# Kernel optimization log

Hardware: AMD Instinct MI355X
Metric: run time of the kernel (lower is better)

Reference implementation:

```python
import jax, jax.numpy as jnp
import numpy as np

HEADS = 8
DIM_HEAD = 32
DIM = 256
HIDDEN = HEADS * DIM_HEAD  # 256


def setup_inputs() -> dict:
    key = jax.random.key(0)
    ks = jax.random.split(key, 6)
    B, T, C, H, W = 4, 16, DIM, 32, 32
    x = jax.random.normal(ks[0], (B, T, C, H, W), dtype=jnp.float32)
    rel_pos = jax.random.normal(ks[1], (HEADS, T, T), dtype=jnp.float32)
    # 1x1 conv weights == channel-mixing matrices
    w_qkv = jax.random.normal(ks[2], (3 * HIDDEN, C), dtype=jnp.float32) * (C ** -0.5)
    b_qkv = jnp.zeros((3 * HIDDEN,), dtype=jnp.float32)
    w_out = jax.random.normal(ks[3], (C, HIDDEN), dtype=jnp.float32) * (HIDDEN ** -0.5)
    b_out = jnp.zeros((C,), dtype=jnp.float32)
    return {"x": x, "rel_pos": rel_pos, "w_qkv": w_qkv, "b_qkv": b_qkv,
            "w_out": w_out, "b_out": b_out}


def reference(x, rel_pos, w_qkv, b_qkv, w_out, b_out):
    B, T, C, H, W = x.shape
    scale = DIM_HEAD ** -0.5
    # 1x1 conv QKV projection: (B,T,C,H,W) x (3*hidden, C) -> (B,T,H,W,3*hidden)
    qkv = jnp.einsum('btchw,oc->bthwo', x, w_qkv) + b_qkv
    q, k, v = jnp.split(qkv, 3, axis=-1)
    # split heads: (B,T,H,W,heads,dim_head); attention over T per (b,h,w,head)
    q = q.reshape(B, T, H, W, HEADS, DIM_HEAD) * scale
    k = k.reshape(B, T, H, W, HEADS, DIM_HEAD)
    v = v.reshape(B, T, H, W, HEADS, DIM_HEAD)
    # sim: (B,H,W,heads,T,T)
    sim = jnp.einsum('bihwnd,bjhwnd->bhwnij', q, k)
    sim = sim + rel_pos  # (heads,T,T) broadcasts over (B,H,W)
    attn = jax.nn.softmax(sim, axis=-1)
    out = jnp.einsum('bhwnij,bjhwnd->bihwnd', attn, v)  # (B,T,H,W,heads,dh)
    out = out.reshape(B, T, H, W, HIDDEN)
    # 1x1 conv output projection back to C channels
    y = jnp.einsum('bthwe,ce->bthwc', out, w_out) + b_out
    return jnp.transpose(y, (0, 1, 4, 2, 3))  # (B,T,C,H,W)
```

## Files before the change

kernel.cpp:

```cpp
#include <hip/hip_runtime.h>
#include <hip/hip_bf16.h>

typedef __attribute__((ext_vector_type(8))) short bf16x8;
typedef __attribute__((ext_vector_type(4))) float f32x4;
typedef __attribute__((ext_vector_type(16))) float f32x16;

namespace {

constexpr int kT = 16;
constexpr int kC = 256;
constexpr int kHW = 1024;

__device__ __forceinline__ unsigned short f2bf(float f) {
  unsigned int x;
  __builtin_memcpy(&x, &f, 4);
  x += 0x7fff + ((x >> 16) & 1);
  return (unsigned short)(x >> 16);
}
__device__ __forceinline__ unsigned int pack2(float a, float b) {
  return (unsigned int)f2bf(a) | ((unsigned int)f2bf(b) << 16);
}

__global__ __launch_bounds__(256) void prep(const float* __restrict__ x,
                                            const float* __restrict__ wqkv,
                                            const float* __restrict__ wout,
                                            unsigned short* __restrict__ xT,
                                            unsigned short* __restrict__ wAll) {
  __shared__ unsigned short ts[64 * 72];
  const int bx = blockIdx.x;
  const int tid = threadIdx.x;
  if (bx < 4096) {
    const int cc = bx & 3, hc = (bx >> 2) & 15, t = (bx >> 6) & 15, b = bx >> 10;
    const int c0 = cc * 64, hw0 = hc * 64;
    {
      const int ci = tid >> 2, j = tid & 3;
      const float* xrow = x + (((size_t)(b * 16 + t) * 256 + c0 + ci) * 1024) + hw0;
#pragma unroll
      for (int u = 0; u < 4; ++u) {
        const int chunk = j + u * 4;
        const float4 v = *(const float4*)(xrow + chunk * 4);
        const int hwl = chunk * 4;
        ts[(hwl + 0) * 72 + ci] = f2bf(v.x);
        ts[(hwl + 1) * 72 + ci] = f2bf(v.y);
        ts[(hwl + 2) * 72 + ci] = f2bf(v.z);
        ts[(hwl + 3) * 72 + ci] = f2bf(v.w);
      }
    }
    __syncthreads();
    {
      const int hwp = tid >> 2, jp = tid & 3;
      const uint4 a = *(const uint4*)&ts[hwp * 72 + jp * 16];
      const uint4 bq = *(const uint4*)&ts[hwp * 72 + jp * 16 + 8];
      unsigned short* dst =
          xT + ((size_t)((b * 1024 + hw0 + hwp) * 16 + t) * 256) + c0 + jp * 16;
      *(uint4*)dst = a;
      *(uint4*)(dst + 8) = bq;
    }
  } else {
    const int g = bx - 4096;
    const int row_l = tid >> 3;
    const int seg = tid & 7;
    const float* src;
    int srow;
    if (g < 24) { src = wqkv; srow = (g % 3) * 256 + (g / 3) * 32 + row_l; }
    else        { src = wout; srow = (g - 24) * 32 + row_l; }
    const float* s = src + (size_t)srow * 256 + seg * 32;
    unsigned short* d = wAll + ((size_t)(g * 32 + row_l)) * 256 + seg * 32;
#pragma unroll
    for (int u = 0; u < 8; ++u) {
      const float4 v = *(const float4*)(s + u * 4);
      uint2 p;
      p.x = pack2(v.x, v.y);
      p.y = pack2(v.z, v.w);
      *(uint2*)(d + u * 4) = p;
    }
  }
}

constexpr int kWBStride = 264;
constexpr int kWBTile = 32 * kWBStride;
constexpr int kWB = 2 * kWBTile;
constexpr int kSite = 1824;
constexpr int kSmem = kWB + 8 * kSite;
static_assert(kSmem * 2 <= 65536, "LDS budget");

__global__ __launch_bounds__(512, 2) void attn_main(
    const unsigned short* __restrict__ xT,
    const float* __restrict__ rel,
    const unsigned short* __restrict__ wAll,
    const float* __restrict__ bqkv,
    const float* __restrict__ bout,
    float* __restrict__ out) {
  __shared__ __align__(16) unsigned short smem[kSmem];
  const int tid = threadIdx.x;
  const int lane = tid & 63;
  const int wave = tid >> 6;
  const int quad = lane >> 4;
  const int lrow = lane & 15;
  const int half = lane >> 5;
  const int n32 = lane & 31;
  const int b = blockIdx.x >> 6;
  const int hw0 = (blockIdx.x & 63) * 16;
  const int site0 = hw0 + wave * 2;

  bf16x8 ax[16];
  {
    const unsigned short* xs =
        xT + (((size_t)(b * 1024 + site0 + (n32 >> 4))) << 12) + lrow * 256;
#pragma unroll
    for (int ks = 0; ks < 16; ++ks)
      ax[ks] = *(const bf16x8*)(xs + ks * 16 + half * 8);
  }

  unsigned short* qb = smem + kWB + wave * kSite;
  unsigned short* kb = qb + 640;
  unsigned short* vt = qb + 1280;

  const int stageDst = (tid >> 4) * kWBStride + (tid & 15) * 16;
  const int stageSrcOff = (tid >> 4) * 256 + (tid & 15) * 16;

  uint4 pr0, pr1;
  {
    const unsigned short* sp = wAll + stageSrcOff;
    pr0 = *(const uint4*)sp;
    pr1 = *(const uint4*)(sp + 8);
  }

  const f32x4 zero4 = {0.f, 0.f, 0.f, 0.f};
  const float scale = 0.17677669529663687f;
  bf16x8 ao[2][8];

  auto qkv_tile = [&](int g, float bias) -> f32x16 {
    __syncthreads();
    unsigned short* WBc = smem + (g & 1) * kWBTile;
    *(uint4*)(WBc + stageDst) = pr0;
    *(uint4*)(WBc + stageDst + 8) = pr1;
    {
      const unsigned short* sp = wAll + (size_t)(g + 1) * 32 * 256 + stageSrcOff;
      pr0 = *(const uint4*)sp;
      pr1 = *(const uint4*)(sp + 8);
    }
    __syncthreads();
    f32x16 acc;
#pragma unroll
    for (int i = 0; i < 16; ++i) acc[i] = bias;
    const unsigned short* br = WBc + n32 * kWBStride + half * 8;
#pragma unroll
    for (int ks = 0; ks < 16; ++ks) {
      const bf16x8 bf = *(const bf16x8*)(br + ks * 16);
      acc = __builtin_amdgcn_mfma_f32_32x32x16_bf16(ax[ks], bf, acc, 0, 0, 0);
    }
    return acc;
  };

#pragma unroll 1
  for (int h = 0; h < 8; ++h) {
    const f32x16 qacc = qkv_tile(h * 3 + 0, bqkv[h * 32 + n32]);
    const f32x16 kacc = qkv_tile(h * 3 + 1, bqkv[256 + h * 32 + n32]);
    const f32x16 vacc = qkv_tile(h * 3 + 2, bqkv[512 + h * 32 + n32]);
    float rl[4];
#pragma unroll
    for (int r = 0; r < 4; ++r) rl[r] = rel[h * 256 + (quad * 4 + r) * 16 + lrow];

#pragma unroll
    for (int s = 0; s < 2; ++s) {
#pragma unroll
      for (int rr = 0; rr < 8; ++rr) {
        const int t = (rr & 3) + 8 * (rr >> 2) + 4 * half;
        qb[t * 40 + n32] = f2bf(qacc[8 * s + rr]);
        kb[t * 40 + n32] = f2bf(kacc[8 * s + rr]);
      }
#pragma unroll
      for (int rp = 0; rp < 4; ++rp) {
        const int rr = rp * 2;
        const int t = (rr & 3) + 8 * (rr >> 2) + 4 * half;
        *(unsigned int*)&vt[n32 * 16 + t] =
            pack2(vacc[8 * s + rr], vacc[8 * s + rr + 1]);
      }
      const bf16x8 qf = *(const bf16x8*)(qb + lrow * 40 + quad * 8);
      const bf16x8 kf = *(const bf16x8*)(kb + lrow * 40 + quad * 8);
      const f32x4 sim = __builtin_amdgcn_mfma_f32_16x16x32_bf16(qf, kf, zero4, 0, 0, 0);
      float p[4], inv[4];
#pragma unroll
      for (int r = 0; r < 4; ++r) {
        const float v = sim[r] * scale + rl[r];
        float m = v;
        for (int off = 8; off; off >>= 1) m = fmaxf(m, __shfl_xor(m, off));
        const float e = __expf(v - m);
        float sum = e;
        for (int off = 8; off; off >>= 1) sum += __shfl_xor(sum, off);
        p[r] = e;
        inv[r] = 1.0f / sum;
      }
      unsigned short* pb = kb;
#pragma unroll
      for (int r = 0; r < 4; ++r) pb[(quad * 4 + r) * 24 + lrow] = f2bf(p[r]);
      bf16x8 pf, vf0, vf1;
      if (quad < 2) {
        pf = *(const bf16x8*)(pb + lrow * 24 + quad * 8);
        vf0 = *(const bf16x8*)(vt + lrow * 16 + quad * 8);
        vf1 = *(const bf16x8*)(vt + (16 + lrow) * 16 + quad * 8);
      } else {
#pragma unroll
        for (int j = 0; j < 8; ++j) { pf[j] = 0; vf0[j] = 0; vf1[j] = 0; }
      }
      const f32x4 o0 = __builtin_amdgcn_mfma_f32_16x16x32_bf16(pf, vf0, zero4, 0, 0, 0);
      const f32x4 o1 = __builtin_amdgcn_mfma_f32_16x16x32_bf16(pf, vf1, zero4, 0, 0, 0);
#pragma unroll
      for (int r = 0; r < 4; ++r) {
        const int t = quad * 4 + r;
        qb[t * 40 + lrow] = f2bf(o0[r] * inv[r]);
        qb[t * 40 + 16 + lrow] = f2bf(o1[r] * inv[r]);
      }
      ao[s][h] = *(const bf16x8*)(qb + lrow * 40 + quad * 8);
    }
  }

  __syncthreads();
  float* fbuf = (float*)smem;
  float* ob = out + ((size_t)b << 22);
#pragma unroll 1
  for (int cc = 0; cc < 8; ++cc) {
#pragma unroll
    for (int sub = 0; sub < 2; ++sub) {
      const int c = cc * 32 + sub * 16 + lrow;
      const float bias = bout[c];
      f32x4 y0 = {bias, bias, bias, bias};
      f32x4 y1 = {bias, bias, bias, bias};
#pragma unroll
      for (int ks = 0; ks < 8; ++ks) {
        const bf16x8 wf =
            *(const bf16x8*)(wAll + (size_t)(768 + c) * 256 + ks * 32 + quad * 8);
        y0 = __builtin_amdgcn_mfma_f32_16x16x32_bf16(ao[0][ks], wf, y0, 0, 0, 0);
        y1 = __builtin_amdgcn_mfma_f32_16x16x32_bf16(ao[1][ks], wf, y1, 0, 0, 0);
      }
#pragma unroll
      for (int r = 0; r < 4; ++r) {
        const int t = quad * 4 + r;
        const int L = (t * 32 + sub * 16 + lrow) * 17 + wave * 2;
        fbuf[L] = y0[r];
        fbuf[L + 1] = y1[r];
      }
    }
    __syncthreads();
    {
      const int t = tid >> 5, cl = tid & 31;
      float v[16];
#pragma unroll
      for (int i = 0; i < 16; ++i) v[i] = fbuf[tid * 17 + i];
      float* dst = ob + ((size_t)(t * 256 + cc * 32 + cl)) * 1024 + hw0;
#pragma unroll
      for (int u = 0; u < 4; ++u) {
        float4 q;
        q.x = v[u * 4]; q.y = v[u * 4 + 1]; q.z = v[u * 4 + 2]; q.w = v[u * 4 + 3];
        *(float4*)(dst + u * 4) = q;
      }
    }
    __syncthreads();
  }
}

constexpr int kHWT = 4;
constexpr int kXsTStride = kC * kHWT + 8;
constexpr int kXSize = kT * kXsTStride;
constexpr int kWsOff = kXSize;
constexpr int kWsStride = 264;
constexpr int kWsSize = 32 * kWsStride;
constexpr int kQbOff = kWsOff + kWsSize;
constexpr int kQbWave = 1792;
constexpr int kLdsElems = kQbOff + 4 * kQbWave;

__global__ __launch_bounds__(256, 2) void fused_temporal_attn(
    const float* __restrict__ x, const float* __restrict__ rel,
    const float* __restrict__ wqkv, const float* __restrict__ bqkv,
    const float* __restrict__ wout, const float* __restrict__ bout,
    float* __restrict__ out) {
  __shared__ __align__(16) unsigned short smem[kLdsElems];
  const int tid = threadIdx.x;
  const int lane = tid & 63;
  const int wave = tid >> 6;
  const int quad = lane >> 4;
  const int lrow = lane & 15;
  const int b = blockIdx.x >> 8;
  const int tile = blockIdx.x & 255;
  const int hw0 = tile * kHWT;
  {
    const float* xb = x + (size_t)b * kT * kC * kHW + hw0;
#pragma unroll
    for (int it = 0; it < 16; ++it) {
      int idx = it * 256 + tid;
      int t = idx >> 8, c = idx & 255;
      const float4 v = *(const float4*)(xb + (size_t)(t * kC + c) * kHW);
      uint2 p;
      p.x = pack2(v.x, v.y);
      p.y = pack2(v.z, v.w);
      *(uint2*)&smem[t * kXsTStride + c * kHWT] = p;
    }
  }
  __syncthreads();
  bf16x8 ax[8];
#pragma unroll
  for (int ks = 0; ks < 8; ++ks) {
    bf16x8 f;
#pragma unroll
    for (int j = 0; j < 8; ++j) {
      int c = ks * 32 + quad * 8 + j;
      f[j] = (short)smem[lrow * kXsTStride + c * kHWT + wave];
    }
    ax[ks] = f;
  }
  unsigned short* qb = &smem[kQbOff + wave * kQbWave];
  unsigned short* kbuf = qb + 512;
  unsigned short* vtb = qb + 1024;
  unsigned short* pb = qb + 1536;
  const f32x4 zero4 = {0.f, 0.f, 0.f, 0.f};
  bf16x8 ao[8];
  for (int head = 0; head < 8; ++head) {
    for (int sel = 0; sel < 3; ++sel) {
      __syncthreads();
      {
        const float* wbp = wqkv + (size_t)(sel * 256 + head * 32) * kC;
#pragma unroll
        for (int i = 0; i < 8; ++i) {
          int seg = i * 256 + tid;
          int d = seg >> 6, s = seg & 63;
          const float4 v = *(const float4*)(wbp + d * kC + s * 4);
          uint2 p;
          p.x = pack2(v.x, v.y);
          p.y = pack2(v.z, v.w);
          *(uint2*)&smem[kWsOff + d * kWsStride + s * 4] = p;
        }
      }
      __syncthreads();
      float bias0 = bqkv[sel * 256 + head * 32 + lrow];
      float bias1 = bqkv[sel * 256 + head * 32 + 16 + lrow];
      f32x4 acc0 = {bias0, bias0, bias0, bias0};
      f32x4 acc1 = {bias1, bias1, bias1, bias1};
#pragma unroll
      for (int ks = 0; ks < 8; ++ks) {
        bf16x8 b0 = *(const bf16x8*)&smem[kWsOff + lrow * kWsStride + ks * 32 + quad * 8];
        bf16x8 b1 = *(const bf16x8*)&smem[kWsOff + (16 + lrow) * kWsStride + ks * 32 + quad * 8];
        acc0 = __builtin_amdgcn_mfma_f32_16x16x32_bf16(ax[ks], b0, acc0, 0, 0, 0);
        acc1 = __builtin_amdgcn_mfma_f32_16x16x32_bf16(ax[ks], b1, acc1, 0, 0, 0);
      }
      if (sel < 2) {
        unsigned short* dst = sel ? kbuf : qb;
#pragma unroll
        for (int r = 0; r < 4; ++r) {
          int row = quad * 4 + r;
          dst[row * 32 + lrow] = f2bf(acc0[r]);
          dst[row * 32 + 16 + lrow] = f2bf(acc1[r]);
        }
      } else {
#pragma unroll
        for (int r = 0; r < 4; ++r) {
          int row = quad * 4 + r;
          vtb[lrow * 16 + row] = f2bf(acc0[r]);
          vtb[(16 + lrow) * 16 + row] = f2bf(acc1[r]);
        }
      }
    }
    bf16x8 qf = *(const bf16x8*)&qb[lrow * 32 + quad * 8];
    bf16x8 kf = *(const bf16x8*)&kbuf[lrow * 32 + quad * 8];
    f32x4 sim = __builtin_amdgcn_mfma_f32_16x16x32_bf16(qf, kf, zero4, 0, 0, 0);
    const float scale = 0.17677669529663687f;
    float p[4], rsum[4];
#pragma unroll
    for (int r = 0; r < 4; ++r) {
      int i = quad * 4 + r;
      float v = sim[r] * scale + rel[head * 256 + i * 16 + lrow];
      float m = v;
      for (int off = 8; off; off >>= 1) m = fmaxf(m, __shfl_xor(m, off));
      float e = __expf(v - m);
      float s = e;
      for (int off = 8; off; off >>= 1) s += __shfl_xor(s, off);
      p[r] = e;
      rsum[r] = s;
    }
#pragma unroll
    for (int r = 0; r < 4; ++r) pb[(quad * 4 + r) * 16 + lrow] = f2bf(p[r]);
    bf16x8 pf, vf0, vf1;
    if (quad < 2) {
      pf = *(const bf16x8*)&pb[lrow * 16 + quad * 8];
      vf0 = *(const bf16x8*)&vtb[lrow * 16 + quad * 8];
      vf1 = *(const bf16x8*)&vtb[(16 + lrow) * 16 + quad * 8];
    } else {
#pragma unroll
      for (int j = 0; j < 8; ++j) { pf[j] = 0; vf0[j] = 0; vf1[j] = 0; }
    }
    f32x4 o0 = __builtin_amdgcn_mfma_f32_16x16x32_bf16(pf, vf0, zero4, 0, 0, 0);
    f32x4 o1 = __builtin_amdgcn_mfma_f32_16x16x32_bf16(pf, vf1, zero4, 0, 0, 0);
#pragma unroll
    for (int r = 0; r < 4; ++r) {
      int t = quad * 4 + r;
      float inv = 1.0f / rsum[r];
      qb[t * 32 + lrow] = f2bf(o0[r] * inv);
      qb[t * 32 + 16 + lrow] = f2bf(o1[r] * inv);
    }
    ao[head] = *(const bf16x8*)&qb[lrow * 32 + quad * 8];
  }
  float* ob = out + (size_t)b * kT * kC * kHW + hw0 + wave;
#pragma unroll 1
  for (int nt = 0; nt < 16; ++nt) {
    int c = nt * 16 + lrow;
    float bias = bout[c];
    f32x4 y = {bias, bias, bias, bias};
#pragma unroll
    for (int ks = 0; ks < 8; ++ks) {
      const float4 w0 = *(const float4*)(wout + (size_t)c * kC + ks * 32 + quad * 8);
      const float4 w1 = *(const float4*)(wout + (size_t)c * kC + ks * 32 + quad * 8 + 4);
      bf16x8 wf;
      wf[0] = (short)f2bf(w0.x); wf[1] = (short)f2bf(w0.y);
      wf[2] = (short)f2bf(w0.z); wf[3] = (short)f2bf(w0.w);
      wf[4] = (short)f2bf(w1.x); wf[5] = (short)f2bf(w1.y);
      wf[6] = (short)f2bf(w1.z); wf[7] = (short)f2bf(w1.w);
      y = __builtin_amdgcn_mfma_f32_16x16x32_bf16(ao[ks], wf, y, 0, 0, 0);
    }
#pragma unroll
    for (int r = 0; r < 4; ++r) {
      int t = quad * 4 + r;
      ob[(size_t)(t * kC + c) * kHW] = y[r];
    }
  }
}

}

extern "C" void kernel_launch(void* const* d_in, const int* in_sizes, int n_in,
                              void* d_out, int out_size, void* d_ws, size_t ws_size,
                              hipStream_t stream) {
  const float* x = (const float*)d_in[0];
  const float* rel = (const float*)d_in[1];
  const float* wqkv = (const float*)d_in[2];
  const float* bqkv = (const float*)d_in[3];
  const float* wout = (const float*)d_in[4];
  const float* bout = (const float*)d_in[5];
  float* out = (float*)d_out;
  (void)in_sizes; (void)n_in; (void)out_size;

  constexpr size_t kXTElems = (size_t)4 * 1024 * 16 * 256;
  constexpr size_t kWAllElems = 1024 * 256;
  constexpr size_t kNeed = (kXTElems + kWAllElems) * sizeof(unsigned short);

  if (ws_size >= kNeed) {
    unsigned short* xT = (unsigned short*)d_ws;
    unsigned short* wAll = xT + kXTElems;
    prep<<<4096 + 32, 256, 0, stream>>>(x, wqkv, wout, xT, wAll);
    attn_main<<<256, 512, 0, stream>>>(xT, rel, wAll, bqkv, bout, out);
  } else {
    fused_temporal_attn<<<1024, 256, 0, stream>>>(x, rel, wqkv, bqkv, wout, bout, out);
  }
}
```

Measured before the change: 243.6 us.

## Halve sites per wave in attn_main, use 16x16 MFMA and nontemporal loads/stores

Each wave now handles one spatial site instead of two, so the grid doubles to 512 blocks and launch bounds request 4 blocks per CU. The QKV projection switches from one 32x32x16 MFMA per k-step to two 16x16x32 MFMAs, which cuts accumulator and fragment register use. The aim is more parallelism and occupancy for a grid that was previously only 256 blocks. Nontemporal loads and stores are also added for the x input, the xT fragments and the output writes. In exchange, each block amortises its weight staging over half as many sites, so weight traffic through LDS doubles, and output stores become 32-byte chunks per row.

```diff
diff --git a/kernel.cpp b/kernel.cpp
--- a/kernel.cpp
+++ b/kernel.cpp
@@ -3,7 +3,7 @@
 
 typedef __attribute__((ext_vector_type(8))) short bf16x8;
 typedef __attribute__((ext_vector_type(4))) float f32x4;
-typedef __attribute__((ext_vector_type(16))) float f32x16;
+typedef __attribute__((ext_vector_type(4))) unsigned int uint4v;
 
 namespace {
 
@@ -19,6 +19,15 @@
 }
 __device__ __forceinline__ unsigned int pack2(float a, float b) {
   return (unsigned int)f2bf(a) | ((unsigned int)f2bf(b) << 16);
+}
+__device__ __forceinline__ bf16x8 ntload8(const unsigned short* p) {
+  uint4v v = __builtin_nontemporal_load((const uint4v*)p);
+  bf16x8 r;
+  __builtin_memcpy(&r, &v, 16);
+  return r;
+}
+__device__ __forceinline__ f32x4 ntload4f(const float* p) {
+  return __builtin_nontemporal_load((const f32x4*)p);
 }
 
 __global__ __launch_bounds__(256) void prep(const float* __restrict__ x,
@@ -38,7 +47,7 @@
 #pragma unroll
       for (int u = 0; u < 4; ++u) {
         const int chunk = j + u * 4;
-        const float4 v = *(const float4*)(xrow + chunk * 4);
+        const f32x4 v = ntload4f(xrow + chunk * 4);
         const int hwl = chunk * 4;
         ts[(hwl + 0) * 72 + ci] = f2bf(v.x);
         ts[(hwl + 1) * 72 + ci] = f2bf(v.y);
@@ -84,7 +93,9 @@
 constexpr int kSmem = kWB + 8 * kSite;
 static_assert(kSmem * 2 <= 65536, "LDS budget");
 
-__global__ __launch_bounds__(512, 2) void attn_main(
+struct Acc2 { f32x4 a0, a1; };
+
+__global__ __launch_bounds__(512, 4) void attn_main(
     const unsigned short* __restrict__ xT,
     const float* __restrict__ rel,
     const unsigned short* __restrict__ wAll,
@@ -97,19 +108,15 @@
   const int wave = tid >> 6;
   const int quad = lane >> 4;
   const int lrow = lane & 15;
-  const int half = lane >> 5;
-  const int n32 = lane & 31;
-  const int b = blockIdx.x >> 6;
-  const int hw0 = (blockIdx.x & 63) * 16;
-  const int site0 = hw0 + wave * 2;
-
-  bf16x8 ax[16];
+  const int b = blockIdx.x >> 7;
+  const int hw0 = (blockIdx.x & 127) * 8;
+  const int site = hw0 + wave;
+
+  bf16x8 ax[8];
   {
-    const unsigned short* xs =
-        xT + (((size_t)(b * 1024 + site0 + (n32 >> 4))) << 12) + lrow * 256;
-#pragma unroll
-    for (int ks = 0; ks < 16; ++ks)
-      ax[ks] = *(const bf16x8*)(xs + ks * 16 + half * 8);
+    const unsigned short* xs = xT + (((size_t)(b * 1024 + site)) << 12) + lrow * 256;
+#pragma unroll
+    for (int ks = 0; ks < 8; ++ks) ax[ks] = ntload8(xs + ks * 32 + quad * 8);
   }
 
   unsigned short* qb = smem + kWB + wave * kSite;
@@ -128,9 +135,9 @@
 
   const f32x4 zero4 = {0.f, 0.f, 0.f, 0.f};
   const float scale = 0.17677669529663687f;
-  bf16x8 ao[2][8];
-
-  auto qkv_tile = [&](int g, float bias) -> f32x16 {
+  bf16x8 ao[8];
+
+  auto qkv_tile = [&](int g, float bias0, float bias1) -> Acc2 {
     __syncthreads();
     unsigned short* WBc = smem + (g & 1) * kWBTile;
     *(uint4*)(WBc + stageDst) = pr0;
@@ -141,79 +148,85 @@
       pr1 = *(const uint4*)(sp + 8);
     }
     __syncthreads();
-    f32x16 acc;
-#pragma unroll
-    for (int i = 0; i < 16; ++i) acc[i] = bias;
-    const unsigned short* br = WBc + n32 * kWBStride + half * 8;
-#pragma unroll
-    for (int ks = 0; ks < 16; ++ks) {
-      const bf16x8 bf = *(const bf16x8*)(br + ks * 16);
-      acc = __builtin_amdgcn_mfma_f32_32x32x16_bf16(ax[ks], bf, acc, 0, 0, 0);
+    Acc2 acc;
+    acc.a0 = f32x4{bias0, bias0, bias0, bias0};
+    acc.a1 = f32x4{bias1, bias1, bias1, bias1};
+    const unsigned short* br0 = WBc + lrow * kWBStride + quad * 8;
+    const unsigned short* br1 = WBc + (16 + lrow) * kWBStride + quad * 8;
+#pragma unroll
+    for (int ks = 0; ks < 8; ++ks) {
+      const bf16x8 b0 = *(const bf16x8*)(br0 + ks * 32);
+      const bf16x8 b1 = *(const bf16x8*)(br1 + ks * 32);
+      acc.a0 = __builtin_amdgcn_mfma_f32_16x16x32_bf16(ax[ks], b0, acc.a0, 0, 0, 0);
+      acc.a1 = __builtin_amdgcn_mfma_f32_16x16x32_bf16(ax[ks], b1, acc.a1, 0, 0, 0);
     }
     return acc;
   };
 
 #pragma unroll 1
   for (int h = 0; h < 8; ++h) {
-    const f32x16 qacc = qkv_tile(h * 3 + 0, bqkv[h * 32 + n32]);
-    const f32x16 kacc = qkv_tile(h * 3 + 1, bqkv[256 + h * 32 + n32]);
-    const f32x16 vacc = qkv_tile(h * 3 + 2, bqkv[512 + h * 32 + n32]);
+    const Acc2 qa = qkv_tile(h * 3 + 0, bqkv[h * 32 + lrow], bqkv[h * 32 + 16 + lrow]);
+    const Acc2 ka = qkv_tile(h * 3 + 1, bqkv[256 + h * 32 + lrow], bqkv[256 + h * 32 + 16 + lrow]);
+    const Acc2 va = qkv_tile(h * 3 + 2, bqkv[512 + h * 32 + lrow], bqkv[512 + h * 32 + 16 + lrow]);
     float rl[4];
 #pragma unroll
     for (int r = 0; r < 4; ++r) rl[r] = rel[h * 256 + (quad * 4 + r) * 16 + lrow];
 
 #pragma unroll
-    for (int s = 0; s < 2; ++s) {
-#pragma unroll
-      for (int rr = 0; rr < 8; ++rr) {
-        const int t = (rr & 3) + 8 * (rr >> 2) + 4 * half;
-        qb[t * 40 + n32] = f2bf(qacc[8 * s + rr]);
-        kb[t * 40 + n32] = f2bf(kacc[8 * s + rr]);
-      }
-#pragma unroll
-      for (int rp = 0; rp < 4; ++rp) {
-        const int rr = rp * 2;
-        const int t = (rr & 3) + 8 * (rr >> 2) + 4 * half;
-        *(unsigned int*)&vt[n32 * 16 + t] =
-            pack2(vacc[8 * s + rr], vacc[8 * s + rr + 1]);
-      }
-      const bf16x8 qf = *(const bf16x8*)(qb + lrow * 40 + quad * 8);
-      const bf16x8 kf = *(const bf16x8*)(kb + lrow * 40 + quad * 8);
-      const f32x4 sim = __builtin_amdgcn_mfma_f32_16x16x32_bf16(qf, kf, zero4, 0, 0, 0);
-      float p[4], inv[4];
-#pragma unroll
-      for (int r = 0; r < 4; ++r) {
-        const float v = sim[r] * scale + rl[r];
-        float m = v;
-        for (int off = 8; off; off >>= 1) m = fmaxf(m, __shfl_xor(m, off));
-        const float e = __expf(v - m);
-        float sum = e;
-        for (int off = 8; off; off >>= 1) sum += __shfl_xor(sum, off);
-        p[r] = e;
-        inv[r] = 1.0f / sum;
-      }
-      unsigned short* pb = kb;
-#pragma unroll
-      for (int r = 0; r < 4; ++r) pb[(quad * 4 + r) * 24 + lrow] = f2bf(p[r]);
-      bf16x8 pf, vf0, vf1;
-      if (quad < 2) {
-        pf = *(const bf16x8*)(pb + lrow * 24 + quad * 8);
-        vf0 = *(const bf16x8*)(vt + lrow * 16 + quad * 8);
-        vf1 = *(const bf16x8*)(vt + (16 + lrow) * 16 + quad * 8);
-      } else {
-#pragma unroll
-        for (int j = 0; j < 8; ++j) { pf[j] = 0; vf0[j] = 0; vf1[j] = 0; }
-      }
-      const f32x4 o0 = __builtin_amdgcn_mfma_f32_16x16x32_bf16(pf, vf0, zero4, 0, 0, 0);
-      const f32x4 o1 = __builtin_amdgcn_mfma_f32_16x16x32_bf16(pf, vf1, zero4, 0, 0, 0);
-#pragma unroll
-      for (int r = 0; r < 4; ++r) {
-        const int t = quad * 4 + r;
-        qb[t * 40 + lrow] = f2bf(o0[r] * inv[r]);
-        qb[t * 40 + 16 + lrow] = f2bf(o1[r] * inv[r]);
-      }
-      ao[s][h] = *(const bf16x8*)(qb + lrow * 40 + quad * 8);
-    }
+    for (int r = 0; r < 4; ++r) {
+      const int row = quad * 4 + r;
+      qb[row * 40 + lrow] = f2bf(qa.a0[r]);
+      qb[row * 40 + 16 + lrow] = f2bf(qa.a1[r]);
+      kb[row * 40 + lrow] = f2bf(ka.a0[r]);
+      kb[row * 40 + 16 + lrow] = f2bf(ka.a1[r]);
+    }
+    {
+      uint2 w0, w1;
+      w0.x = pack2(va.a0[0], va.a0[1]);
+      w0.y = pack2(va.a0[2], va.a0[3]);
+      w1.x = pack2(va.a1[0], va.a1[1]);
+      w1.y = pack2(va.a1[2], va.a1[3]);
+      *(uint2*)&vt[lrow * 16 + quad * 4] = w0;
+      *(uint2*)&vt[(16 + lrow) * 16 + quad * 4] = w1;
+    }
+
+    const bf16x8 qf = *(const bf16x8*)(qb + lrow * 40 + quad * 8);
+    const bf16x8 kf = *(const bf16x8*)(kb + lrow * 40 + quad * 8);
+    const f32x4 sim = __builtin_amdgcn_mfma_f32_16x16x32_bf16(qf, kf, zero4, 0, 0, 0);
+    float p[4], inv[4];
+#pragma unroll
+    for (int r = 0; r < 4; ++r) {
+      const float v = sim[r] * scale + rl[r];
+      float m = v;
+      for (int off = 8; off; off >>= 1) m = fmaxf(m, __shfl_xor(m, off));
+      const float e = __expf(v - m);
+      float sum = e;
+      for (int off = 8; off; off >>= 1) sum += __shfl_xor(sum, off);
+      p[r] = e;
+      inv[r] = 1.0f / sum;
+    }
+    unsigned short* pb = kb;
+#pragma unroll
+    for (int r = 0; r < 4; ++r) pb[(quad * 4 + r) * 24 + lrow] = f2bf(p[r]);
+
+    bf16x8 pf, vf0, vf1;
+    if (quad < 2) {
+      pf = *(const bf16x8*)(pb + lrow * 24 + quad * 8);
+      vf0 = *(const bf16x8*)(vt + lrow * 16 + quad * 8);
+      vf1 = *(const bf16x8*)(vt + (16 + lrow) * 16 + quad * 8);
+    } else {
+#pragma unroll
+      for (int j = 0; j < 8; ++j) { pf[j] = 0; vf0[j] = 0; vf1[j] = 0; }
+    }
+    const f32x4 o0 = __builtin_amdgcn_mfma_f32_16x16x32_bf16(pf, vf0, zero4, 0, 0, 0);
+    const f32x4 o1 = __builtin_amdgcn_mfma_f32_16x16x32_bf16(pf, vf1, zero4, 0, 0, 0);
+#pragma unroll
+    for (int r = 0; r < 4; ++r) {
+      const int t = quad * 4 + r;
+      qb[t * 40 + lrow] = f2bf(o0[r] * inv[r]);
+      qb[t * 40 + 16 + lrow] = f2bf(o1[r] * inv[r]);
+    }
+    ao[h] = *(const bf16x8*)(qb + lrow * 40 + quad * 8);
   }
 
   __syncthreads();
@@ -225,36 +238,31 @@
     for (int sub = 0; sub < 2; ++sub) {
       const int c = cc * 32 + sub * 16 + lrow;
       const float bias = bout[c];
-      f32x4 y0 = {bias, bias, bias, bias};
-      f32x4 y1 = {bias, bias, bias, bias};
+      f32x4 y = {bias, bias, bias, bias};
 #pragma unroll
       for (int ks = 0; ks < 8; ++ks) {
         const bf16x8 wf =
             *(const bf16x8*)(wAll + (size_t)(768 + c) * 256 + ks * 32 + quad * 8);
-        y0 = __builtin_amdgcn_mfma_f32_16x16x32_bf16(ao[0][ks], wf, y0, 0, 0, 0);
-        y1 = __builtin_amdgcn_mfma_f32_16x16x32_bf16(ao[1][ks], wf, y1, 0, 0, 0);
+        y = __builtin_amdgcn_mfma_f32_16x16x32_bf16(ao[ks], wf, y, 0, 0, 0);
       }
 #pragma unroll
       for (int r = 0; r < 4; ++r) {
         const int t = quad * 4 + r;
-        const int L = (t * 32 + sub * 16 + lrow) * 17 + wave * 2;
-        fbuf[L] = y0[r];
-        fbuf[L + 1] = y1[r];
+        fbuf[(t * 32 + sub * 16 + lrow) * 9 + wave] = y[r];
       }
     }
     __syncthreads();
     {
       const int t = tid >> 5, cl = tid & 31;
-      float v[16];
-#pragma unroll
-      for (int i = 0; i < 16; ++i) v[i] = fbuf[tid * 17 + i];
+      float v[8];
+#pragma unroll
+      for (int i = 0; i < 8; ++i) v[i] = fbuf[tid * 9 + i];
       float* dst = ob + ((size_t)(t * 256 + cc * 32 + cl)) * 1024 + hw0;
-#pragma unroll
-      for (int u = 0; u < 4; ++u) {
-        float4 q;
-        q.x = v[u * 4]; q.y = v[u * 4 + 1]; q.z = v[u * 4 + 2]; q.w = v[u * 4 + 3];
-        *(float4*)(dst + u * 4) = q;
-      }
+      f32x4 q0, q1;
+      q0.x = v[0]; q0.y = v[1]; q0.z = v[2]; q0.w = v[3];
+      q1.x = v[4]; q1.y = v[5]; q1.z = v[6]; q1.w = v[7];
+      __builtin_nontemporal_store(q0, (f32x4*)dst);
+      __builtin_nontemporal_store(q1, (f32x4*)(dst + 4));
     }
     __syncthreads();
   }
@@ -446,7 +454,7 @@
     unsigned short* xT = (unsigned short*)d_ws;
     unsigned short* wAll = xT + kXTElems;
     prep<<<4096 + 32, 256, 0, stream>>>(x, wqkv, wout, xT, wAll);
-    attn_main<<<256, 512, 0, stream>>>(xT, rel, wAll, bqkv, bout, out);
+    attn_main<<<512, 512, 0, stream>>>(xT, rel, wAll, bqkv, bout, out);
   } else {
     fused_temporal_attn<<<1024, 256, 0, stream>>>(x, rel, wqkv, bqkv, wout, bout, out);
   }
```

After: 454.1 us. 86.4% more time.
